# Optimization experiments

Measured on AMD Instinct MI355X. Metric: run time of the kernel, lower is better.

The kernel has to match this reference:

```python
import jax, jax.numpy as jnp
import numpy as np


def setup_inputs() -> dict:
    key = jax.random.key(0)
    kq, kk, kv = jax.random.split(key, 3)
    B, H, S, D = 4, 16, 2048, 64
    q = jax.random.normal(kq, (B, H, S, D), dtype=jnp.float32)
    k = jax.random.normal(kk, (B, H, S, D), dtype=jnp.float32)
    v = jax.random.normal(kv, (B, H, S, D), dtype=jnp.float32)
    return {"q": q, "k": k, "v": v}


def reference(q, k, v):
    # scale = sqrt(d_k); source's self.scale is undefined, standard SDPA scaling assumed
    scale = jnp.asarray(np.sqrt(q.shape[-1]), dtype=q.dtype)
    # [B,H,S,S] scores; sigmoid instead of softmax (no normalization across keys)
    scores = jnp.einsum("bhqd,bhkd->bhqk", q, k) / scale
    attn = jax.nn.sigmoid(scores)
    return jnp.einsum("bhqk,bhkd->bhqd", attn, v)
```

## Files before the change

kernel.cpp:

```cpp
#include <hip/hip_runtime.h>


typedef __bf16 bf16_t;
typedef __attribute__((ext_vector_type(8))) __bf16 bf16x8;
typedef __attribute__((ext_vector_type(4))) __bf16 bf16x4;
typedef __attribute__((ext_vector_type(4))) float  f32x4;

#if defined(__HIP_DEVICE_COMPILE__) && __has_builtin(__builtin_amdgcn_exp2f)
#define FAST_EXP2(x) __builtin_amdgcn_exp2f(x)
#else
#define FAST_EXP2(x) exp2f(x)
#endif
#if defined(__HIP_DEVICE_COMPILE__) && __has_builtin(__builtin_amdgcn_rcpf)
#define FAST_RCP(x) __builtin_amdgcn_rcpf(x)
#else
#define FAST_RCP(x) (1.0f/(x))
#endif

static constexpr int SEQ = 2048;
static constexpr int DH  = 64;
static constexpr int KB  = 32;
static constexpr int NIT = SEQ / KB;
static constexpr int QPW = 32;
static constexpr int QPB = 128;
static constexpr int CHUNK = 4096;

__global__ __launch_bounds__(256)
void sigattn_prepass(const float* __restrict__ Kg, const float* __restrict__ Vg,
                     bf16_t* __restrict__ ws)
{
    const int bh = blockIdx.x, it = blockIdx.y;
    const int t  = threadIdx.x;
    const int kb = it * KB;
    const size_t hbase = (size_t)bh * SEQ * DH;
    bf16_t* wbase = ws + ((size_t)bh * NIT + it) * CHUNK;

    {
        const int f = t >> 6, lane = t & 63;
        const int ks = f >> 1, dh = f & 1, c16 = lane & 15, g4 = lane >> 4;
        const float* p = Kg + hbase + (size_t)(kb + ks * 16 + c16) * DH + dh * 32 + g4 * 8;
        f32x4 a = *(const f32x4*)p;
        f32x4 b = *(const f32x4*)(p + 4);
        bf16x8 o;
        o[0] = (bf16_t)a.x; o[1] = (bf16_t)a.y; o[2] = (bf16_t)a.z; o[3] = (bf16_t)a.w;
        o[4] = (bf16_t)b.x; o[5] = (bf16_t)b.y; o[6] = (bf16_t)b.z; o[7] = (bf16_t)b.w;
        *(bf16x8*)&wbase[(size_t)t * 8] = o;
    }
    {
        const int c = t & 63, rblk = t >> 6;
        const int dt = c >> 4, c16 = c & 15;
        const float* p = Vg + hbase + (size_t)(kb + rblk * 8) * DH + c;
        float v[8];
        #pragma unroll
        for (int i = 0; i < 8; ++i) v[i] = p[(size_t)i * DH];
        const int j0  = (rblk >> 1) * 4;
        const int g4a = (rblk & 1) * 2;
        bf16x4 ca, cb;
        #pragma unroll
        for (int i = 0; i < 4; ++i) { ca[i] = (bf16_t)v[i]; cb[i] = (bf16_t)v[4 + i]; }
        bf16_t* vr = wbase + 2048;
        *(bf16x4*)&vr[(size_t)(dt * 64 + g4a * 16 + c16) * 8 + j0]       = ca;
        *(bf16x4*)&vr[(size_t)(dt * 64 + (g4a + 1) * 16 + c16) * 8 + j0] = cb;
    }
}

__global__ __launch_bounds__(256, 4)
void sigattn_main(const float* __restrict__ Qg, const bf16_t* __restrict__ ws,
                  float* __restrict__ Og)
{
    __shared__ __align__(16) bf16_t buf[2][CHUNK];

    const int t    = threadIdx.x;
    const int wave = t >> 6;
    const int lane = t & 63;
    const int c16  = lane & 15;
    const int g4   = lane >> 4;

    const int bh    = blockIdx.x;
    const int qtile = blockIdx.y;

    const float* Qp = Qg + (size_t)bh * SEQ * DH;
    float*       Op = Og + (size_t)bh * SEQ * DH;
    const bf16_t* wsh = ws + (size_t)bh * NIT * CHUNK;

    const int qwave = qtile * QPB + wave * QPW;

    const float qscale = -0.125f * 1.44269504088896340736f;
    bf16x8 qf[2][2];
    #pragma unroll
    for (int qs = 0; qs < 2; ++qs) {
        #pragma unroll
        for (int dh = 0; dh < 2; ++dh) {
            const float* p = Qp + (size_t)(qwave + qs * 16 + c16) * DH + dh * 32 + g4 * 8;
            f32x4 a = *(const f32x4*)p;
            f32x4 b = *(const f32x4*)(p + 4);
            bf16x8 f;
            f[0] = (bf16_t)(a.x * qscale); f[1] = (bf16_t)(a.y * qscale);
            f[2] = (bf16_t)(a.z * qscale); f[3] = (bf16_t)(a.w * qscale);
            f[4] = (bf16_t)(b.x * qscale); f[5] = (bf16_t)(b.y * qscale);
            f[6] = (bf16_t)(b.z * qscale); f[7] = (bf16_t)(b.w * qscale);
            qf[qs][dh] = f;
        }
    }

    bf16x8 rK, rV;
    auto gload = [&](int it) {
        const bf16_t* g = wsh + (size_t)it * CHUNK + t * 8;
        rK = *(const bf16x8*)g;
        rV = *(const bf16x8*)(g + 2048);
    };
    auto lstore = [&](int nb) {
        *(bf16x8*)&buf[nb][t * 8]        = rK;
        *(bf16x8*)&buf[nb][2048 + t * 8] = rV;
    };

    gload(0);
    lstore(0);

    f32x4 acc[2][4] = {};

    for (int it = 0; it < NIT; ++it) {
        const int cur = it & 1;
        __syncthreads();
        if (it + 1 < NIT) gload(it + 1);

        bf16x8 kf[4], vf[4];
        #pragma unroll
        for (int f = 0; f < 4; ++f) kf[f] = *(const bf16x8*)&buf[cur][(f * 64 + lane) * 8];
        #pragma unroll
        for (int f = 0; f < 4; ++f) vf[f] = *(const bf16x8*)&buf[cur][2048 + (f * 64 + lane) * 8];

        #pragma unroll
        for (int qs = 0; qs < 2; ++qs) {
            f32x4 s0 = {0.f, 0.f, 0.f, 0.f}, s1 = {0.f, 0.f, 0.f, 0.f};
            s0 = __builtin_amdgcn_mfma_f32_16x16x32_bf16(kf[0], qf[qs][0], s0, 0, 0, 0);
            s0 = __builtin_amdgcn_mfma_f32_16x16x32_bf16(kf[1], qf[qs][1], s0, 0, 0, 0);
            s1 = __builtin_amdgcn_mfma_f32_16x16x32_bf16(kf[2], qf[qs][0], s1, 0, 0, 0);
            s1 = __builtin_amdgcn_mfma_f32_16x16x32_bf16(kf[3], qf[qs][1], s1, 0, 0, 0);
            bf16x8 p8;
            #pragma unroll
            for (int r = 0; r < 4; ++r) p8[r]     = (bf16_t)FAST_RCP(1.0f + FAST_EXP2(s0[r]));
            #pragma unroll
            for (int r = 0; r < 4; ++r) p8[4 + r] = (bf16_t)FAST_RCP(1.0f + FAST_EXP2(s1[r]));
            #pragma unroll
            for (int dt = 0; dt < 4; ++dt)
                acc[qs][dt] = __builtin_amdgcn_mfma_f32_16x16x32_bf16(p8, vf[dt], acc[qs][dt], 0, 0, 0);
        }

        if (it + 1 < NIT) lstore(cur ^ 1);
    }

    #pragma unroll
    for (int qs = 0; qs < 2; ++qs) {
        const int q0 = qwave + qs * 16 + g4 * 4;
        #pragma unroll
        for (int r = 0; r < 4; ++r) {
            float* po = Op + (size_t)(q0 + r) * DH + c16;
            po[0]  = acc[qs][0][r];
            po[16] = acc[qs][1][r];
            po[32] = acc[qs][2][r];
            po[48] = acc[qs][3][r];
        }
    }
}

__global__ __launch_bounds__(256, 4)
void sigattn_fallback(const float* __restrict__ Qg, const float* __restrict__ Kg,
                      const float* __restrict__ Vg, float* __restrict__ Og)
{
    __shared__ bf16_t Kbuf[2][4 * 64 * 8];
    __shared__ bf16_t Vbuf[2][4 * 64 * 8];
    const int t = threadIdx.x, wave = t >> 6, lane = t & 63;
    const int c16 = lane & 15, g4 = lane >> 4;
    const int bh = blockIdx.x, qtile = blockIdx.y;
    const size_t hbase = (size_t)bh * SEQ * DH;
    const float* Qp = Qg + hbase; const float* Kp = Kg + hbase;
    const float* Vp = Vg + hbase; float* Op = Og + hbase;
    const int qwave = qtile * QPB + wave * QPW;
    const float qscale = -0.125f * 1.44269504088896340736f;
    bf16x8 qf[2][2];
    #pragma unroll
    for (int qs = 0; qs < 2; ++qs)
        #pragma unroll
        for (int dh = 0; dh < 2; ++dh) {
            const float* p = Qp + (size_t)(qwave + qs * 16 + c16) * DH + dh * 32 + g4 * 8;
            f32x4 a = *(const f32x4*)p; f32x4 b = *(const f32x4*)(p + 4);
            bf16x8 f;
            f[0]=(bf16_t)(a.x*qscale); f[1]=(bf16_t)(a.y*qscale); f[2]=(bf16_t)(a.z*qscale); f[3]=(bf16_t)(a.w*qscale);
            f[4]=(bf16_t)(b.x*qscale); f[5]=(bf16_t)(b.y*qscale); f[6]=(bf16_t)(b.z*qscale); f[7]=(bf16_t)(b.w*qscale);
            qf[qs][dh] = f;
        }
    f32x4 kst0, kst1; float vst[8];
    auto issue_loads = [&](int kb0) {
        const float* pk = Kp + (size_t)(kb0 + (wave >> 1) * 16 + c16) * DH + (wave & 1) * 32 + g4 * 8;
        kst0 = *(const f32x4*)pk; kst1 = *(const f32x4*)(pk + 4);
        const float* pv = Vp + (size_t)(kb0 + g4 * 4) * DH + wave * 16 + c16;
        #pragma unroll
        for (int h = 0; h < 2; ++h)
            #pragma unroll
            for (int j = 0; j < 4; ++j) vst[h * 4 + j] = pv[(size_t)(h * 16 + j) * DH];
    };
    auto store_lds = [&](int buf) {
        bf16x8 k8;
        k8[0]=(bf16_t)kst0.x; k8[1]=(bf16_t)kst0.y; k8[2]=(bf16_t)kst0.z; k8[3]=(bf16_t)kst0.w;
        k8[4]=(bf16_t)kst1.x; k8[5]=(bf16_t)kst1.y; k8[6]=(bf16_t)kst1.z; k8[7]=(bf16_t)kst1.w;
        *(bf16x8*)&Kbuf[buf][t * 8] = k8;
        bf16x8 v8;
        #pragma unroll
        for (int j = 0; j < 8; ++j) v8[j] = (bf16_t)vst[j];
        *(bf16x8*)&Vbuf[buf][t * 8] = v8;
    };
    issue_loads(0); store_lds(0);
    f32x4 acc[2][4] = {};
    for (int it = 0; it < NIT; ++it) {
        const int buf = it & 1;
        __syncthreads();
        if (it + 1 < NIT) issue_loads((it + 1) * KB);
        bf16x8 kf[4], vf[4];
        #pragma unroll
        for (int f = 0; f < 4; ++f) kf[f] = *(const bf16x8*)&Kbuf[buf][(f * 64 + lane) * 8];
        #pragma unroll
        for (int f = 0; f < 4; ++f) vf[f] = *(const bf16x8*)&Vbuf[buf][(f * 64 + lane) * 8];
        #pragma unroll
        for (int qs = 0; qs < 2; ++qs) {
            f32x4 s0 = {0.f,0.f,0.f,0.f}, s1 = {0.f,0.f,0.f,0.f};
            s0 = __builtin_amdgcn_mfma_f32_16x16x32_bf16(kf[0], qf[qs][0], s0, 0, 0, 0);
            s0 = __builtin_amdgcn_mfma_f32_16x16x32_bf16(kf[1], qf[qs][1], s0, 0, 0, 0);
            s1 = __builtin_amdgcn_mfma_f32_16x16x32_bf16(kf[2], qf[qs][0], s1, 0, 0, 0);
            s1 = __builtin_amdgcn_mfma_f32_16x16x32_bf16(kf[3], qf[qs][1], s1, 0, 0, 0);
            bf16x8 p8;
            #pragma unroll
            for (int r = 0; r < 4; ++r) p8[r]     = (bf16_t)FAST_RCP(1.0f + FAST_EXP2(s0[r]));
            #pragma unroll
            for (int r = 0; r < 4; ++r) p8[4 + r] = (bf16_t)FAST_RCP(1.0f + FAST_EXP2(s1[r]));
            #pragma unroll
            for (int dt = 0; dt < 4; ++dt)
                acc[qs][dt] = __builtin_amdgcn_mfma_f32_16x16x32_bf16(p8, vf[dt], acc[qs][dt], 0, 0, 0);
        }
        if (it + 1 < NIT) store_lds(buf ^ 1);
    }
    #pragma unroll
    for (int qs = 0; qs < 2; ++qs) {
        const int q0 = qwave + qs * 16 + g4 * 4;
        #pragma unroll
        for (int r = 0; r < 4; ++r) {
            float* po = Op + (size_t)(q0 + r) * DH + c16;
            po[0]  = acc[qs][0][r];
            po[16] = acc[qs][1][r];
            po[32] = acc[qs][2][r];
            po[48] = acc[qs][3][r];
        }
    }
}

extern "C" void kernel_launch(void* const* d_in, const int* in_sizes, int n_in,
                              void* d_out, int out_size, void* d_ws, size_t ws_size,
                              hipStream_t stream)
{
    const float* q = (const float*)d_in[0];
    const float* k = (const float*)d_in[1];
    const float* v = (const float*)d_in[2];
    float* o = (float*)d_out;
    const size_t need = 64ull * NIT * CHUNK * sizeof(bf16_t);
    if (ws_size >= need) {
        sigattn_prepass<<<dim3(64, NIT), dim3(256), 0, stream>>>(k, v, (bf16_t*)d_ws);
        sigattn_main<<<dim3(64, SEQ / QPB), dim3(256), 0, stream>>>(q, (const bf16_t*)d_ws, o);
    } else {
        sigattn_fallback<<<dim3(64, SEQ / QPB), dim3(256), 0, stream>>>(q, k, v, o);
    }
}
```

Baseline: 204.0 us.

## Double K/V chunk per pipeline stage, add MFMA priority hints, rework V prepass

The main loop now stages two 32-key chunks per iteration, so LDS grows to 32 KB and there are half as many barriers and global-to-LDS handoffs. It wraps the MFMA groups in s_setprio to favour matrix issue across the waves sharing a SIMD. The V prepass is rewritten so each thread gathers eight strided rows and writes one contiguous bf16x8, which should produce the same packed layout with fewer, wider stores. The costs are more registers for the prefetch and more LDS per block, which may lower occupancy under launch_bounds(256,4).

```diff
diff --git a/kernel.cpp b/kernel.cpp
--- a/kernel.cpp
+++ b/kernel.cpp
@@ -21,6 +21,7 @@
 static constexpr int DH  = 64;
 static constexpr int KB  = 32;
 static constexpr int NIT = SEQ / KB;
+static constexpr int NIT2 = NIT / 2;
 static constexpr int QPW = 32;
 static constexpr int QPB = 128;
 static constexpr int CHUNK = 4096;
@@ -47,20 +48,16 @@
         *(bf16x8*)&wbase[(size_t)t * 8] = o;
     }
     {
-        const int c = t & 63, rblk = t >> 6;
-        const int dt = c >> 4, c16 = c & 15;
-        const float* p = Vg + hbase + (size_t)(kb + rblk * 8) * DH + c;
-        float v[8];
-        #pragma unroll
-        for (int i = 0; i < 8; ++i) v[i] = p[(size_t)i * DH];
-        const int j0  = (rblk >> 1) * 4;
-        const int g4a = (rblk & 1) * 2;
-        bf16x4 ca, cb;
-        #pragma unroll
-        for (int i = 0; i < 4; ++i) { ca[i] = (bf16_t)v[i]; cb[i] = (bf16_t)v[4 + i]; }
-        bf16_t* vr = wbase + 2048;
-        *(bf16x4*)&vr[(size_t)(dt * 64 + g4a * 16 + c16) * 8 + j0]       = ca;
-        *(bf16x4*)&vr[(size_t)(dt * 64 + (g4a + 1) * 16 + c16) * 8 + j0] = cb;
+        const int lane = t & 63, dt = t >> 6;
+        const int c16 = lane & 15, g4 = lane >> 4;
+        const float* p = Vg + hbase + (size_t)kb * DH + dt * 16 + c16;
+        bf16x8 o;
+        #pragma unroll
+        for (int j = 0; j < 8; ++j) {
+            const int row = (j >> 2) * 16 + g4 * 4 + (j & 3);
+            o[j] = (bf16_t)p[(size_t)row * DH];
+        }
+        *(bf16x8*)&wbase[2048 + (size_t)t * 8] = o;
     }
 }
 
@@ -68,7 +65,7 @@
 void sigattn_main(const float* __restrict__ Qg, const bf16_t* __restrict__ ws,
                   float* __restrict__ Og)
 {
-    __shared__ __align__(16) bf16_t buf[2][CHUNK];
+    __shared__ __align__(16) bf16_t buf[2][2 * CHUNK];
 
     const int t    = threadIdx.x;
     const int wave = t >> 6;
@@ -103,51 +100,63 @@
         }
     }
 
-    bf16x8 rK, rV;
-    auto gload = [&](int it) {
-        const bf16_t* g = wsh + (size_t)it * CHUNK + t * 8;
-        rK = *(const bf16x8*)g;
-        rV = *(const bf16x8*)(g + 2048);
-    };
-    auto lstore = [&](int nb) {
-        *(bf16x8*)&buf[nb][t * 8]        = rK;
-        *(bf16x8*)&buf[nb][2048 + t * 8] = rV;
-    };
-
-    gload(0);
-    lstore(0);
+    bf16x8 rK0, rV0, rK1, rV1;
+    auto gload2 = [&](int su) {
+        const bf16_t* g = wsh + (size_t)(2 * su) * CHUNK + t * 8;
+        rK0 = *(const bf16x8*)g;
+        rV0 = *(const bf16x8*)(g + 2048);
+        rK1 = *(const bf16x8*)(g + CHUNK);
+        rV1 = *(const bf16x8*)(g + CHUNK + 2048);
+    };
+    auto lstore2 = [&](int nb) {
+        *(bf16x8*)&buf[nb][t * 8]                = rK0;
+        *(bf16x8*)&buf[nb][2048 + t * 8]         = rV0;
+        *(bf16x8*)&buf[nb][CHUNK + t * 8]        = rK1;
+        *(bf16x8*)&buf[nb][CHUNK + 2048 + t * 8] = rV1;
+    };
+
+    gload2(0);
+    lstore2(0);
 
     f32x4 acc[2][4] = {};
 
-    for (int it = 0; it < NIT; ++it) {
-        const int cur = it & 1;
+    for (int su = 0; su < NIT2; ++su) {
+        const int cur = su & 1;
         __syncthreads();
-        if (it + 1 < NIT) gload(it + 1);
-
-        bf16x8 kf[4], vf[4];
-        #pragma unroll
-        for (int f = 0; f < 4; ++f) kf[f] = *(const bf16x8*)&buf[cur][(f * 64 + lane) * 8];
-        #pragma unroll
-        for (int f = 0; f < 4; ++f) vf[f] = *(const bf16x8*)&buf[cur][2048 + (f * 64 + lane) * 8];
-
-        #pragma unroll
-        for (int qs = 0; qs < 2; ++qs) {
-            f32x4 s0 = {0.f, 0.f, 0.f, 0.f}, s1 = {0.f, 0.f, 0.f, 0.f};
-            s0 = __builtin_amdgcn_mfma_f32_16x16x32_bf16(kf[0], qf[qs][0], s0, 0, 0, 0);
-            s0 = __builtin_amdgcn_mfma_f32_16x16x32_bf16(kf[1], qf[qs][1], s0, 0, 0, 0);
-            s1 = __builtin_amdgcn_mfma_f32_16x16x32_bf16(kf[2], qf[qs][0], s1, 0, 0, 0);
-            s1 = __builtin_amdgcn_mfma_f32_16x16x32_bf16(kf[3], qf[qs][1], s1, 0, 0, 0);
-            bf16x8 p8;
-            #pragma unroll
-            for (int r = 0; r < 4; ++r) p8[r]     = (bf16_t)FAST_RCP(1.0f + FAST_EXP2(s0[r]));
-            #pragma unroll
-            for (int r = 0; r < 4; ++r) p8[4 + r] = (bf16_t)FAST_RCP(1.0f + FAST_EXP2(s1[r]));
-            #pragma unroll
-            for (int dt = 0; dt < 4; ++dt)
-                acc[qs][dt] = __builtin_amdgcn_mfma_f32_16x16x32_bf16(p8, vf[dt], acc[qs][dt], 0, 0, 0);
-        }
-
-        if (it + 1 < NIT) lstore(cur ^ 1);
+        if (su + 1 < NIT2) gload2(su + 1);
+
+        #pragma unroll
+        for (int h = 0; h < 2; ++h) {
+            const bf16_t* base = &buf[cur][h * CHUNK];
+            bf16x8 kf[4], vf[4];
+            #pragma unroll
+            for (int f = 0; f < 4; ++f) kf[f] = *(const bf16x8*)&base[(f * 64 + lane) * 8];
+            #pragma unroll
+            for (int f = 0; f < 4; ++f) vf[f] = *(const bf16x8*)&base[2048 + (f * 64 + lane) * 8];
+
+            #pragma unroll
+            for (int qs = 0; qs < 2; ++qs) {
+                f32x4 s0 = {0.f, 0.f, 0.f, 0.f}, s1 = {0.f, 0.f, 0.f, 0.f};
+                __builtin_amdgcn_s_setprio(1);
+                s0 = __builtin_amdgcn_mfma_f32_16x16x32_bf16(kf[0], qf[qs][0], s0, 0, 0, 0);
+                s0 = __builtin_amdgcn_mfma_f32_16x16x32_bf16(kf[1], qf[qs][1], s0, 0, 0, 0);
+                s1 = __builtin_amdgcn_mfma_f32_16x16x32_bf16(kf[2], qf[qs][0], s1, 0, 0, 0);
+                s1 = __builtin_amdgcn_mfma_f32_16x16x32_bf16(kf[3], qf[qs][1], s1, 0, 0, 0);
+                __builtin_amdgcn_s_setprio(0);
+                bf16x8 p8;
+                #pragma unroll
+                for (int r = 0; r < 4; ++r) p8[r]     = (bf16_t)FAST_RCP(1.0f + FAST_EXP2(s0[r]));
+                #pragma unroll
+                for (int r = 0; r < 4; ++r) p8[4 + r] = (bf16_t)FAST_RCP(1.0f + FAST_EXP2(s1[r]));
+                __builtin_amdgcn_s_setprio(1);
+                #pragma unroll
+                for (int dt = 0; dt < 4; ++dt)
+                    acc[qs][dt] = __builtin_amdgcn_mfma_f32_16x16x32_bf16(p8, vf[dt], acc[qs][dt], 0, 0, 0);
+                __builtin_amdgcn_s_setprio(0);
+            }
+        }
+
+        if (su + 1 < NIT2) lstore2(cur ^ 1);
     }
 
     #pragma unroll
```

After: 208.3 us. +2.1%, slower.
